# Kernel tuning notes

Measured on AMD Instinct MI355X. Metric: run time of the kernel, lower is better.

The kernel has to match this reference:

```python
import jax, jax.numpy as jnp
import numpy as np

B, D, H, V, T = 64, 1024, 1024, 32000, 20
SOS = 0  # word_to_idx['<SOS>']


def setup_inputs() -> dict:
    key = jax.random.key(0)
    ks = jax.random.split(key, 6)
    s = 0.02
    return {
        "latent_vector": jax.random.normal(ks[0], (B, D), jnp.float32),
        "W_proj": jax.random.normal(ks[1], (H, D), jnp.float32) * s,
        "b_proj": jnp.zeros((H,), jnp.float32),
        "emb": jax.random.normal(ks[2], (V, H), jnp.float32) * s,
        "W_ih": jax.random.normal(ks[3], (3 * H, H), jnp.float32) * s,
        "b_ih": jnp.zeros((3 * H,), jnp.float32),
        "W_hh": jax.random.normal(ks[4], (3 * H, H), jnp.float32) * s,
        "b_hh": jnp.zeros((3 * H,), jnp.float32),
        "W_out": jax.random.normal(ks[5], (V, H), jnp.float32) * s,
        "b_out": jnp.zeros((V,), jnp.float32),
    }


def _gru_cell(x, h, W_ih, b_ih, W_hh, b_hh):
    # PyTorch GRU cell gate math
    gi = x @ W_ih.T + b_ih  # [B, 3H]
    gh = h @ W_hh.T + b_hh  # [B, 3H]
    i_r, i_z, i_n = jnp.split(gi, 3, axis=-1)
    h_r, h_z, h_n = jnp.split(gh, 3, axis=-1)
    r = jax.nn.sigmoid(i_r + h_r)
    z = jax.nn.sigmoid(i_z + h_z)
    n = jnp.tanh(i_n + r * h_n)
    return (1.0 - z) * n + z * h


def reference(latent_vector, W_proj, b_proj, emb, W_ih, b_ih, W_hh, b_hh, W_out, b_out):
    batch = latent_vector.shape[0]
    h = latent_vector @ W_proj.T + b_proj  # init_hidden: [B, H]
    tok0 = jnp.full((batch,), SOS, dtype=jnp.int32)

    def step(carry, _):
        tok, h = carry
        x = emb[tok]                                  # embedding lookup [B, H]
        h = _gru_cell(x, h, W_ih, b_ih, W_hh, b_hh)   # GRU step
        logits = h @ W_out.T + b_out                  # [B, V]
        tok = jnp.argmax(logits, axis=-1).astype(jnp.int32)  # topk(1) greedy
        return (tok, h), tok

    (_, h_final), toks = jax.lax.scan(step, (tok0, h), None, length=T)
    # torch: stack(outputs, dim=1).squeeze() -> [B, T]; hidden -> [1, B, H]
    return toks.T, h_final[None, :, :]
```

## Files before the change

### kernel.cpp

```cpp
#include <hip/hip_runtime.h>
#include <stdint.h>

#define B_ 64
#define D_ 1024
#define H_ 1024
#define V_ 32000
#define T_ 20
#define SOS_ 0

typedef __attribute__((ext_vector_type(8))) __bf16 bf16x8;
typedef __attribute__((ext_vector_type(4))) float f32x4;

__device__ __forceinline__ uint32_t ord_of_float(float x) {
    uint32_t u = __float_as_uint(x);
    return (u & 0x80000000u) ? ~u : (u | 0x80000000u);
}

__device__ __forceinline__ unsigned long long shfl_xor_u64(unsigned long long x, int m) {
    return (unsigned long long)__shfl_xor((long long)x, m, 64);
}

__device__ __forceinline__ void split_bf16(float f, unsigned short* hi, unsigned short* lo) {
    uint32_t u = __float_as_uint(f);
    uint32_t rh = (u + 0x7FFFu + ((u >> 16) & 1u)) >> 16;
    *hi = (unsigned short)rh;
    float fl = f - __uint_as_float(rh << 16);
    uint32_t ul = __float_as_uint(fl);
    uint32_t rl = (ul + 0x7FFFu + ((ul >> 16) & 1u)) >> 16;
    *lo = (unsigned short)rl;
}

__device__ __forceinline__ void gload_lds16(const void* g, void* l) {
    __builtin_amdgcn_global_load_lds(
        (const __attribute__((address_space(1))) void*)g,
        (__attribute__((address_space(3))) void*)l, 16, 0, 0);
}

__global__ __launch_bounds__(256) void k_split_w(const float* __restrict__ src,
    unsigned short* __restrict__ hi, unsigned short* __restrict__ lo, int n4)
{
    int i = blockIdx.x * 256 + threadIdx.x;
    if (i >= n4) return;
    float4 v = ((const float4*)src)[i];
    ushort4 h, l;
    split_bf16(v.x, &h.x, &l.x);
    split_bf16(v.y, &h.y, &l.y);
    split_bf16(v.z, &h.z, &l.z);
    split_bf16(v.w, &h.w, &l.w);
    ((ushort4*)hi)[i] = h;
    ((ushort4*)lo)[i] = l;
}

__global__ __launch_bounds__(256) void k_init_hidden(
    const float* __restrict__ latent, const float* __restrict__ Wp,
    const float* __restrict__ bp, float* __restrict__ h0,
    unsigned short* __restrict__ hhi, unsigned short* __restrict__ hlo)
{
    int gw = (blockIdx.x * 256 + threadIdx.x) >> 6;
    int lane = threadIdx.x & 63;
    int j = gw >> 6;
    int b = gw & 63;
    const float4* a4 = (const float4*)(latent + b * D_);
    const float4* w4 = (const float4*)(Wp + (size_t)j * D_);
    float s = 0.f;
#pragma unroll
    for (int i = 0; i < 4; i++) {
        float4 a = a4[lane + 64 * i];
        float4 w = w4[lane + 64 * i];
        s += a.x * w.x + a.y * w.y + a.z * w.z + a.w * w.w;
    }
#pragma unroll
    for (int off = 32; off; off >>= 1) s += __shfl_down(s, off, 64);
    if (lane == 0) {
        float v = s + bp[j];
        h0[b * H_ + j] = v;
        unsigned short h_, l_;
        split_bf16(v, &h_, &l_);
        hhi[b * H_ + j] = h_;
        hlo[b * H_ + j] = l_;
    }
}

__global__ __launch_bounds__(256) void k_prep_x0(const float* __restrict__ emb,
    unsigned short* __restrict__ xhi, unsigned short* __restrict__ xlo)
{
    int b = blockIdx.x;
    int tid = threadIdx.x;
    float4 v4 = *(const float4*)(emb + (size_t)SOS_ * H_ + tid * 4);
    ushort4 h, l;
    split_bf16(v4.x, &h.x, &l.x);
    split_bf16(v4.y, &h.y, &l.y);
    split_bf16(v4.z, &h.z, &l.z);
    split_bf16(v4.w, &h.w, &l.w);
    *(ushort4*)(xhi + (size_t)b * H_ + tid * 4) = h;
    *(ushort4*)(xlo + (size_t)b * H_ + tid * 4) = l;
}

__global__ __launch_bounds__(256) void k_gates_gemm2(
    const unsigned short* __restrict__ xhi, const unsigned short* __restrict__ xlo,
    const unsigned short* __restrict__ hhi, const unsigned short* __restrict__ hlo,
    const unsigned short* __restrict__ wihh, const unsigned short* __restrict__ wihl,
    const unsigned short* __restrict__ whhh, const unsigned short* __restrict__ whhl,
    float* __restrict__ gbuf)
{
    __shared__ __align__(128) char Bsm[4][16384];
    int tid = threadIdx.x;
    int lane = tid & 63;
    int wv = tid >> 6;
    int blk = blockIdx.x;
    int jt = blk % 48;
    int rest = blk / 48;
    int half = rest & 1;
    int ks = rest >> 1;
    int kbase = ks * 256;
    int row0 = jt * 64;

    const unsigned short* Ahi_g = half ? hhi : xhi;
    const unsigned short* Alo_g = half ? hlo : xlo;
    const unsigned short* Bhi_g = half ? whhh : wihh;
    const unsigned short* Blo_g = half ? whhl : wihl;

    int r0 = wv * 8 + (lane >> 3);
    int r1 = r0 + 32;
    int kslt = (lane & 7) * 16;
    size_t so0 = (size_t)(row0 + r0) * 2048 + (size_t)(kslt ^ ((r0 & 7) << 4));
    size_t so1 = (size_t)(row0 + r1) * 2048 + (size_t)(kslt ^ ((r1 & 7) << 4));

    int mrow = wv * 16 + (lane & 15);
    int koff = (lane >> 4) * 8;
    int kb = koff * 2;

    f32x4 acc[4];
#pragma unroll
    for (int i = 0; i < 4; i++) acc[i] = (f32x4){0.f, 0.f, 0.f, 0.f};

    bf16x8 AH0[4], AH1[4], AL0[4], AL1[4];
#pragma unroll
    for (int it = 0; it < 4; it++) {
        int kc = kbase + it * 64;
        const unsigned short* ap  = Ahi_g + (size_t)mrow * 1024 + kc + koff;
        const unsigned short* alp = Alo_g + (size_t)mrow * 1024 + kc + koff;
        AH0[it] = *(const bf16x8*)ap;
        AH1[it] = *(const bf16x8*)(ap + 32);
        AL0[it] = *(const bf16x8*)alp;
        AL1[it] = *(const bf16x8*)(alp + 32);
    }
    __builtin_amdgcn_sched_barrier(0);

    auto stage = [&](int BUF, int KC) {
        const char* bh = (const char*)Bhi_g + (size_t)KC * 2;
        const char* bl = (const char*)Blo_g + (size_t)KC * 2;
        char* base = Bsm[BUF] + wv * 1024;
        gload_lds16(bh + so0, base);
        gload_lds16(bh + so1, base + 4096);
        gload_lds16(bl + so0, base + 8192);
        gload_lds16(bl + so1, base + 12288);
    };

    stage(0, kbase);
    stage(1, kbase + 64);
    stage(2, kbase + 128);
    stage(3, kbase + 192);
    __builtin_amdgcn_sched_barrier(0);

#pragma unroll
    for (int it = 0; it < 4; ++it) {
        if (it == 0)      asm volatile("s_waitcnt vmcnt(12)" ::: "memory");
        else if (it == 1) asm volatile("s_waitcnt vmcnt(8)"  ::: "memory");
        else if (it == 2) asm volatile("s_waitcnt vmcnt(4)"  ::: "memory");
        else              asm volatile("s_waitcnt vmcnt(0)"  ::: "memory");
        __builtin_amdgcn_s_barrier();
        __builtin_amdgcn_sched_barrier(0);
        const char* bhp = Bsm[it];
        const char* blp = Bsm[it] + 8192;
#pragma unroll
        for (int tv = 0; tv < 4; tv++) {
            int brow = tv * 16 + (lane & 15);
            int swz = (brow & 7) << 4;
            int ro = brow * 128;
            bf16x8 bh0 = *(const bf16x8*)(bhp + ro + (kb ^ swz));
            bf16x8 bh1 = *(const bf16x8*)(bhp + ro + ((kb + 64) ^ swz));
            bf16x8 bl0 = *(const bf16x8*)(blp + ro + (kb ^ swz));
            bf16x8 bl1 = *(const bf16x8*)(blp + ro + ((kb + 64) ^ swz));
            acc[tv] = __builtin_amdgcn_mfma_f32_16x16x32_bf16(AH0[it], bh0, acc[tv], 0, 0, 0);
            acc[tv] = __builtin_amdgcn_mfma_f32_16x16x32_bf16(AH1[it], bh1, acc[tv], 0, 0, 0);
            acc[tv] = __builtin_amdgcn_mfma_f32_16x16x32_bf16(AL0[it], bh0, acc[tv], 0, 0, 0);
            acc[tv] = __builtin_amdgcn_mfma_f32_16x16x32_bf16(AL1[it], bh1, acc[tv], 0, 0, 0);
            acc[tv] = __builtin_amdgcn_mfma_f32_16x16x32_bf16(AH0[it], bl0, acc[tv], 0, 0, 0);
            acc[tv] = __builtin_amdgcn_mfma_f32_16x16x32_bf16(AH1[it], bl1, acc[tv], 0, 0, 0);
        }
    }

    int col = lane & 15;
    int quad = lane >> 4;
    float* og = gbuf + (size_t)((ks * 2 + half) * 64) * 3072;
#pragma unroll
    for (int tv = 0; tv < 4; tv++) {
#pragma unroll
        for (int r = 0; r < 4; r++) {
            int b = wv * 16 + quad * 4 + r;
            og[(size_t)b * 3072 + jt * 64 + tv * 16 + col] = acc[tv][r];
        }
    }
}

__global__ __launch_bounds__(256) void k_gru_elem2(
    const float* __restrict__ gbuf, const float* __restrict__ bih,
    const float* __restrict__ bhh, const float* __restrict__ hprev,
    float* __restrict__ hnext, unsigned short* __restrict__ hnhi,
    unsigned short* __restrict__ hnlo)
{
    int idx = blockIdx.x * 256 + threadIdx.x;
    int b = idx >> 10;
    int j = idx & 1023;
    float ir = bih[j], hr = bhh[j];
    float iz = bih[H_ + j], hz = bhh[H_ + j];
    float in_ = bih[2 * H_ + j], hn = bhh[2 * H_ + j];
#pragma unroll
    for (int ks = 0; ks < 4; ks++) {
        const float* gi = gbuf + (size_t)(ks * 2 * 64 + b) * 3072;
        const float* gh = gbuf + (size_t)((ks * 2 + 1) * 64 + b) * 3072;
        ir += gi[j];          hr += gh[j];
        iz += gi[H_ + j];     hz += gh[H_ + j];
        in_ += gi[2 * H_ + j]; hn += gh[2 * H_ + j];
    }
    float r = 1.f / (1.f + expf(-(ir + hr)));
    float z = 1.f / (1.f + expf(-(iz + hz)));
    float n = tanhf(in_ + r * hn);
    float hp = hprev[idx];
    float v = (1.f - z) * n + z * hp;
    hnext[idx] = v;
    unsigned short h_, l_;
    split_bf16(v, &h_, &l_);
    hnhi[idx] = h_;
    hnlo[idx] = l_;
}

__global__ __launch_bounds__(256) void k_logits_argmax2(
    const unsigned short* __restrict__ hhi, const unsigned short* __restrict__ hlo,
    const unsigned short* __restrict__ wouth, const unsigned short* __restrict__ woutl,
    const float* __restrict__ bout, unsigned long long* __restrict__ partials,
    int nblk)
{
    __shared__ __align__(128) char Bsm[4][16384];
    int tid = threadIdx.x;
    int lane = tid & 63;
    int wv = tid >> 6;
    int row0 = blockIdx.x * 64;

    int r0 = wv * 8 + (lane >> 3);
    int r1 = r0 + 32;
    int kslt = (lane & 7) * 16;
    size_t so0 = (size_t)(row0 + r0) * 2048 + (size_t)(kslt ^ ((r0 & 7) << 4));
    size_t so1 = (size_t)(row0 + r1) * 2048 + (size_t)(kslt ^ ((r1 & 7) << 4));

    int mrow = wv * 16 + (lane & 15);
    int koff = (lane >> 4) * 8;
    int kb = koff * 2;

    f32x4 acc[4];
#pragma unroll
    for (int i = 0; i < 4; i++) acc[i] = (f32x4){0.f, 0.f, 0.f, 0.f};

    auto stage = [&](int BUF, int KC) {
        const char* bh = (const char*)wouth + (size_t)KC * 2;
        const char* bl = (const char*)woutl + (size_t)KC * 2;
        char* base = Bsm[BUF] + wv * 1024;
        gload_lds16(bh + so0, base);
        gload_lds16(bh + so1, base + 4096);
        gload_lds16(bl + so0, base + 8192);
        gload_lds16(bl + so1, base + 12288);
    };

    struct AF { bf16x8 h0, h1, l0, l1; };
    auto loadA = [&](int kc) {
        AF f;
        const unsigned short* ap  = hhi + (size_t)mrow * 1024 + kc + koff;
        const unsigned short* alp = hlo + (size_t)mrow * 1024 + kc + koff;
        f.h0 = *(const bf16x8*)ap;
        f.h1 = *(const bf16x8*)(ap + 32);
        f.l0 = *(const bf16x8*)alp;
        f.l1 = *(const bf16x8*)(alp + 32);
        return f;
    };
    auto mmaBlk = [&](const AF& a, const char* bhp, const char* blp) {
#pragma unroll
        for (int tv = 0; tv < 4; tv++) {
            int brow = tv * 16 + (lane & 15);
            int swz = (brow & 7) << 4;
            int ro = brow * 128;
            bf16x8 bh0 = *(const bf16x8*)(bhp + ro + (kb ^ swz));
            bf16x8 bh1 = *(const bf16x8*)(bhp + ro + ((kb + 64) ^ swz));
            bf16x8 bl0 = *(const bf16x8*)(blp + ro + (kb ^ swz));
            bf16x8 bl1 = *(const bf16x8*)(blp + ro + ((kb + 64) ^ swz));
            acc[tv] = __builtin_amdgcn_mfma_f32_16x16x32_bf16(a.h0, bh0, acc[tv], 0, 0, 0);
            acc[tv] = __builtin_amdgcn_mfma_f32_16x16x32_bf16(a.h1, bh1, acc[tv], 0, 0, 0);
            acc[tv] = __builtin_amdgcn_mfma_f32_16x16x32_bf16(a.l0, bh0, acc[tv], 0, 0, 0);
            acc[tv] = __builtin_amdgcn_mfma_f32_16x16x32_bf16(a.l1, bh1, acc[tv], 0, 0, 0);
            acc[tv] = __builtin_amdgcn_mfma_f32_16x16x32_bf16(a.h0, bl0, acc[tv], 0, 0, 0);
            acc[tv] = __builtin_amdgcn_mfma_f32_16x16x32_bf16(a.h1, bl1, acc[tv], 0, 0, 0);
        }
    };

    stage(0, 0);
    stage(1, 64);
    stage(2, 128);
    __builtin_amdgcn_sched_barrier(0);
    AF Ae = loadA(0);
    AF Ao;
    __builtin_amdgcn_sched_barrier(0);

    for (int it2 = 0; it2 < 16; it2 += 2) {
        if (it2 == 0 || it2 == 14) asm volatile("s_waitcnt vmcnt(0)" ::: "memory");
        else                       asm volatile("s_waitcnt vmcnt(4)" ::: "memory");
        __builtin_amdgcn_s_barrier();
        __builtin_amdgcn_sched_barrier(0);
        Ao = loadA((it2 + 1) * 64);
        __builtin_amdgcn_sched_barrier(0);
        if (it2 <= 12) stage((it2 + 3) & 3, (it2 + 3) * 64);
        __builtin_amdgcn_sched_barrier(0);
        mmaBlk(Ae, Bsm[it2 & 3], Bsm[it2 & 3] + 8192);

        if (it2 + 1 >= 14) asm volatile("s_waitcnt vmcnt(0)" ::: "memory");
        else               asm volatile("s_waitcnt vmcnt(4)" ::: "memory");
        __builtin_amdgcn_s_barrier();
        __builtin_amdgcn_sched_barrier(0);
        if (it2 + 2 < 16) Ae = loadA((it2 + 2) * 64);
        __builtin_amdgcn_sched_barrier(0);
        if (it2 + 1 <= 12) stage((it2 + 4) & 3, (it2 + 4) * 64);
        __builtin_amdgcn_sched_barrier(0);
        mmaBlk(Ao, Bsm[(it2 + 1) & 3], Bsm[(it2 + 1) & 3] + 8192);
    }

    int col = lane & 15;
    int quad = lane >> 4;
    unsigned long long kmax[4] = {0ull, 0ull, 0ull, 0ull};
#pragma unroll
    for (int tv = 0; tv < 4; tv++) {
        int v = row0 + tv * 16 + col;
        float bo = bout[v];
#pragma unroll
        for (int r = 0; r < 4; r++) {
            float lg = acc[tv][r] + bo;
            unsigned long long key = ((unsigned long long)ord_of_float(lg) << 32)
                                   | (unsigned long long)(0x7FFFFFFFu - (uint32_t)v);
            if (key > kmax[r]) kmax[r] = key;
        }
    }
#pragma unroll
    for (int r = 0; r < 4; r++) {
        unsigned long long k = kmax[r];
#pragma unroll
        for (int off = 1; off < 16; off <<= 1) {
            unsigned long long o = shfl_xor_u64(k, off);
            if (o > k) k = o;
        }
        kmax[r] = k;
    }
    if (col == 0) {
#pragma unroll
        for (int r = 0; r < 4; r++) {
            int b = wv * 16 + quad * 4 + r;
            partials[(size_t)b * nblk + blockIdx.x] = kmax[r];
        }
    }
}

__global__ __launch_bounds__(256) void k_token2(
    const unsigned long long* __restrict__ partials, int nblk,
    int* __restrict__ tok, float* __restrict__ out_tokens, int t,
    const float* __restrict__ emb,
    unsigned short* __restrict__ xhi, unsigned short* __restrict__ xlo)
{
    __shared__ int s_tok;
    int b = blockIdx.x;
    int tid = threadIdx.x;
    if (tid < 64) {
        unsigned long long k = 0ull;
        for (int i = tid; i < nblk; i += 64) {
            unsigned long long p = partials[(size_t)b * nblk + i];
            if (p > k) k = p;
        }
#pragma unroll
        for (int off = 32; off; off >>= 1) {
            unsigned long long o = shfl_xor_u64(k, off);
            if (o > k) k = o;
        }
        if (tid == 0) {
            int v = (int)(0x7FFFFFFFu - (uint32_t)(k & 0xFFFFFFFFull));
            tok[b] = v;
            out_tokens[b * T_ + t] = (float)v;
            s_tok = v;
        }
    }
    __syncthreads();
    int row = s_tok;
    float4 v4 = *(const float4*)(emb + (size_t)row * H_ + tid * 4);
    ushort4 h, l;
    split_bf16(v4.x, &h.x, &l.x);
    split_bf16(v4.y, &h.y, &l.y);
    split_bf16(v4.z, &h.z, &l.z);
    split_bf16(v4.w, &h.w, &l.w);
    *(ushort4*)(xhi + (size_t)b * H_ + tid * 4) = h;
    *(ushort4*)(xlo + (size_t)b * H_ + tid * 4) = l;
}

__global__ __launch_bounds__(256) void k_copy_h(const float* __restrict__ h,
                                               float* __restrict__ out)
{
    int i = (blockIdx.x * 256 + threadIdx.x) * 4;
    *(float4*)(out + i) = *(const float4*)(h + i);
}

extern "C" void kernel_launch(void* const* d_in, const int* in_sizes, int n_in,
                              void* d_out, int out_size, void* d_ws, size_t ws_size,
                              hipStream_t stream)
{
    const float* latent = (const float*)d_in[0];
    const float* Wp     = (const float*)d_in[1];
    const float* bp     = (const float*)d_in[2];
    const float* emb    = (const float*)d_in[3];
    const float* Wih    = (const float*)d_in[4];
    const float* bih    = (const float*)d_in[5];
    const float* Whh    = (const float*)d_in[6];
    const float* bhh    = (const float*)d_in[7];
    const float* Wout   = (const float*)d_in[8];
    const float* bout   = (const float*)d_in[9];
    float* out = (float*)d_out;

    char* ws = (char*)d_ws;
    float* h0   = (float*)(ws + 0);
    float* h1   = (float*)(ws + 262144);
    int* tok    = (int*)(ws + 524288);
    unsigned long long* partials = (unsigned long long*)(ws + 525312);
    float* gbuf = (float*)(ws + 787456);
    unsigned short* hhi0 = (unsigned short*)(ws + 7078912);
    unsigned short* hlo0 = (unsigned short*)(ws + 7209984);
    unsigned short* hhi1 = (unsigned short*)(ws + 7341056);
    unsigned short* hlo1 = (unsigned short*)(ws + 7472128);
    unsigned short* xhi  = (unsigned short*)(ws + 7603200);
    unsigned short* xlo  = (unsigned short*)(ws + 7734272);
    unsigned short* wihh = (unsigned short*)(ws + 7865344);
    unsigned short* wihl = (unsigned short*)(ws + 14156800);
    unsigned short* whhh = (unsigned short*)(ws + 20448256);
    unsigned short* whhl = (unsigned short*)(ws + 26739712);
    unsigned short* wouth = (unsigned short*)(ws + 33031168);
    unsigned short* woutl = (unsigned short*)(ws + 98567168);

    const int NBLK = V_ / 64;

    k_split_w<<<3072, 256, 0, stream>>>(Wih, wihh, wihl, 3 * H_ * H_ / 4);
    k_split_w<<<3072, 256, 0, stream>>>(Whh, whhh, whhl, 3 * H_ * H_ / 4);
    k_split_w<<<32000, 256, 0, stream>>>(Wout, wouth, woutl, V_ * H_ / 4);

    k_init_hidden<<<16384, 256, 0, stream>>>(latent, Wp, bp, h0, hhi0, hlo0);
    k_prep_x0<<<64, 256, 0, stream>>>(emb, xhi, xlo);

    float* hp = h0;  unsigned short* hphi = hhi0;  unsigned short* hplo = hlo0;
    float* hn = h1;  unsigned short* hnhi = hhi1;  unsigned short* hnlo = hlo1;
    for (int t = 0; t < T_; t++) {
        k_gates_gemm2<<<384, 256, 0, stream>>>(xhi, xlo, hphi, hplo,
                                               wihh, wihl, whhh, whhl, gbuf);
        k_gru_elem2<<<256, 256, 0, stream>>>(gbuf, bih, bhh, hp, hn, hnhi, hnlo);
        k_logits_argmax2<<<NBLK, 256, 0, stream>>>(hnhi, hnlo, wouth, woutl,
                                                   bout, partials, NBLK);
        k_token2<<<B_, 256, 0, stream>>>(partials, NBLK, tok, out, t, emb, xhi, xlo);
        { float* tf = hp; hp = hn; hn = tf; }
        { unsigned short* ts = hphi; hphi = hnhi; hnhi = ts; }
        { unsigned short* ts = hplo; hplo = hnlo; hnlo = ts; }
    }
    k_copy_h<<<64, 256, 0, stream>>>(hp, out + B_ * T_);
}
```

Baseline: 1.185 ms.

## Fuse GRU gate GEMM with elementwise update via permuted weight layout; MFMA init projection

```diff
diff --git a/kernel.cpp b/kernel.cpp
--- a/kernel.cpp
+++ b/kernel.cpp
@@ -51,34 +51,24 @@
     ((ushort4*)lo)[i] = l;
 }
 
-__global__ __launch_bounds__(256) void k_init_hidden(
-    const float* __restrict__ latent, const float* __restrict__ Wp,
-    const float* __restrict__ bp, float* __restrict__ h0,
-    unsigned short* __restrict__ hhi, unsigned short* __restrict__ hlo)
-{
-    int gw = (blockIdx.x * 256 + threadIdx.x) >> 6;
-    int lane = threadIdx.x & 63;
-    int j = gw >> 6;
-    int b = gw & 63;
-    const float4* a4 = (const float4*)(latent + b * D_);
-    const float4* w4 = (const float4*)(Wp + (size_t)j * D_);
-    float s = 0.f;
-#pragma unroll
-    for (int i = 0; i < 4; i++) {
-        float4 a = a4[lane + 64 * i];
-        float4 w = w4[lane + 64 * i];
-        s += a.x * w.x + a.y * w.y + a.z * w.z + a.w * w.w;
-    }
-#pragma unroll
-    for (int off = 32; off; off >>= 1) s += __shfl_down(s, off, 64);
-    if (lane == 0) {
-        float v = s + bp[j];
-        h0[b * H_ + j] = v;
-        unsigned short h_, l_;
-        split_bf16(v, &h_, &l_);
-        hhi[b * H_ + j] = h_;
-        hlo[b * H_ + j] = l_;
-    }
+__global__ __launch_bounds__(256) void k_split_w_perm(const float* __restrict__ src,
+    unsigned short* __restrict__ hi, unsigned short* __restrict__ lo)
+{
+    int rp = blockIdx.x;
+    int jt = rp / 48;
+    int rem = rp % 48;
+    int g = rem >> 4;
+    int jl = rem & 15;
+    int orig = g * H_ + jt * 16 + jl;
+    int c4 = threadIdx.x * 4;
+    float4 v = *(const float4*)(src + (size_t)orig * H_ + c4);
+    ushort4 h, l;
+    split_bf16(v.x, &h.x, &l.x);
+    split_bf16(v.y, &h.y, &l.y);
+    split_bf16(v.z, &h.z, &l.z);
+    split_bf16(v.w, &h.w, &l.w);
+    *(ushort4*)(hi + (size_t)rp * H_ + c4) = h;
+    *(ushort4*)(lo + (size_t)rp * H_ + c4) = l;
 }
 
 __global__ __launch_bounds__(256) void k_prep_x0(const float* __restrict__ emb,
@@ -96,29 +86,17 @@
     *(ushort4*)(xlo + (size_t)b * H_ + tid * 4) = l;
 }
 
-__global__ __launch_bounds__(256) void k_gates_gemm2(
-    const unsigned short* __restrict__ xhi, const unsigned short* __restrict__ xlo,
-    const unsigned short* __restrict__ hhi, const unsigned short* __restrict__ hlo,
-    const unsigned short* __restrict__ wihh, const unsigned short* __restrict__ wihl,
-    const unsigned short* __restrict__ whhh, const unsigned short* __restrict__ whhl,
-    float* __restrict__ gbuf)
+__global__ __launch_bounds__(256) void k_init_gemm(
+    const unsigned short* __restrict__ lathi, const unsigned short* __restrict__ latlo,
+    const unsigned short* __restrict__ wphi, const unsigned short* __restrict__ wplo,
+    const float* __restrict__ bp, float* __restrict__ h0,
+    unsigned short* __restrict__ hhi, unsigned short* __restrict__ hlo)
 {
     __shared__ __align__(128) char Bsm[4][16384];
     int tid = threadIdx.x;
     int lane = tid & 63;
     int wv = tid >> 6;
-    int blk = blockIdx.x;
-    int jt = blk % 48;
-    int rest = blk / 48;
-    int half = rest & 1;
-    int ks = rest >> 1;
-    int kbase = ks * 256;
-    int row0 = jt * 64;
-
-    const unsigned short* Ahi_g = half ? hhi : xhi;
-    const unsigned short* Alo_g = half ? hlo : xlo;
-    const unsigned short* Bhi_g = half ? whhh : wihh;
-    const unsigned short* Blo_g = half ? whhl : wihl;
+    int row0 = blockIdx.x * 64;
 
     int r0 = wv * 8 + (lane >> 3);
     int r1 = r0 + 32;
@@ -134,22 +112,9 @@
 #pragma unroll
     for (int i = 0; i < 4; i++) acc[i] = (f32x4){0.f, 0.f, 0.f, 0.f};
 
-    bf16x8 AH0[4], AH1[4], AL0[4], AL1[4];
-#pragma unroll
-    for (int it = 0; it < 4; it++) {
-        int kc = kbase + it * 64;
-        const unsigned short* ap  = Ahi_g + (size_t)mrow * 1024 + kc + koff;
-        const unsigned short* alp = Alo_g + (size_t)mrow * 1024 + kc + koff;
-        AH0[it] = *(const bf16x8*)ap;
-        AH1[it] = *(const bf16x8*)(ap + 32);
-        AL0[it] = *(const bf16x8*)alp;
-        AL1[it] = *(const bf16x8*)(alp + 32);
-    }
-    __builtin_amdgcn_sched_barrier(0);
-
     auto stage = [&](int BUF, int KC) {
-        const char* bh = (const char*)Bhi_g + (size_t)KC * 2;
-        const char* bl = (const char*)Blo_g + (size_t)KC * 2;
+        const char* bh = (const char*)wphi + (size_t)KC * 2;
+        const char* bl = (const char*)wplo + (size_t)KC * 2;
         char* base = Bsm[BUF] + wv * 1024;
         gload_lds16(bh + so0, base);
         gload_lds16(bh + so1, base + 4096);
@@ -157,22 +122,25 @@
         gload_lds16(bl + so1, base + 12288);
     };
 
-    stage(0, kbase);
-    stage(1, kbase + 64);
-    stage(2, kbase + 128);
-    stage(3, kbase + 192);
-    __builtin_amdgcn_sched_barrier(0);
-
-#pragma unroll
-    for (int it = 0; it < 4; ++it) {
-        if (it == 0)      asm volatile("s_waitcnt vmcnt(12)" ::: "memory");
-        else if (it == 1) asm volatile("s_waitcnt vmcnt(8)"  ::: "memory");
-        else if (it == 2) asm volatile("s_waitcnt vmcnt(4)"  ::: "memory");
-        else              asm volatile("s_waitcnt vmcnt(0)"  ::: "memory");
+    stage(0, 0);
+    stage(1, 64);
+    stage(2, 128);
+
+    for (int it = 0; it < 16; ++it) {
+        if (it == 0)      asm volatile("s_waitcnt vmcnt(8)"  ::: "memory");
+        else if (it == 1) asm volatile("s_waitcnt vmcnt(12)" ::: "memory");
+        else              asm volatile("s_waitcnt vmcnt(16)" ::: "memory");
         __builtin_amdgcn_s_barrier();
         __builtin_amdgcn_sched_barrier(0);
-        const char* bhp = Bsm[it];
-        const char* blp = Bsm[it] + 8192;
+        int kc = it * 64;
+        const unsigned short* ap  = lathi + (size_t)mrow * 1024 + kc + koff;
+        const unsigned short* alp = latlo + (size_t)mrow * 1024 + kc + koff;
+        bf16x8 ah0 = *(const bf16x8*)ap;
+        bf16x8 ah1 = *(const bf16x8*)(ap + 32);
+        bf16x8 al0 = *(const bf16x8*)alp;
+        bf16x8 al1 = *(const bf16x8*)(alp + 32);
+        const char* bhp = Bsm[it & 3];
+        const char* blp = Bsm[it & 3] + 8192;
 #pragma unroll
         for (int tv = 0; tv < 4; tv++) {
             int brow = tv * 16 + (lane & 15);
@@ -182,58 +150,167 @@
             bf16x8 bh1 = *(const bf16x8*)(bhp + ro + ((kb + 64) ^ swz));
             bf16x8 bl0 = *(const bf16x8*)(blp + ro + (kb ^ swz));
             bf16x8 bl1 = *(const bf16x8*)(blp + ro + ((kb + 64) ^ swz));
-            acc[tv] = __builtin_amdgcn_mfma_f32_16x16x32_bf16(AH0[it], bh0, acc[tv], 0, 0, 0);
-            acc[tv] = __builtin_amdgcn_mfma_f32_16x16x32_bf16(AH1[it], bh1, acc[tv], 0, 0, 0);
-            acc[tv] = __builtin_amdgcn_mfma_f32_16x16x32_bf16(AL0[it], bh0, acc[tv], 0, 0, 0);
-            acc[tv] = __builtin_amdgcn_mfma_f32_16x16x32_bf16(AL1[it], bh1, acc[tv], 0, 0, 0);
-            acc[tv] = __builtin_amdgcn_mfma_f32_16x16x32_bf16(AH0[it], bl0, acc[tv], 0, 0, 0);
-            acc[tv] = __builtin_amdgcn_mfma_f32_16x16x32_bf16(AH1[it], bl1, acc[tv], 0, 0, 0);
-        }
+            acc[tv] = __builtin_amdgcn_mfma_f32_16x16x32_bf16(ah0, bh0, acc[tv], 0, 0, 0);
+            acc[tv] = __builtin_amdgcn_mfma_f32_16x16x32_bf16(ah1, bh1, acc[tv], 0, 0, 0);
+            acc[tv] = __builtin_amdgcn_mfma_f32_16x16x32_bf16(al0, bh0, acc[tv], 0, 0, 0);
+            acc[tv] = __builtin_amdgcn_mfma_f32_16x16x32_bf16(al1, bh1, acc[tv], 0, 0, 0);
+            acc[tv] = __builtin_amdgcn_mfma_f32_16x16x32_bf16(ah0, bl0, acc[tv], 0, 0, 0);
+            acc[tv] = __builtin_amdgcn_mfma_f32_16x16x32_bf16(ah1, bl1, acc[tv], 0, 0, 0);
+        }
+        if (it <= 12) stage((it + 3) & 3, (it + 3) * 64);
     }
 
     int col = lane & 15;
     int quad = lane >> 4;
-    float* og = gbuf + (size_t)((ks * 2 + half) * 64) * 3072;
 #pragma unroll
     for (int tv = 0; tv < 4; tv++) {
+        int j = row0 + tv * 16 + col;
+        float bo = bp[j];
 #pragma unroll
         for (int r = 0; r < 4; r++) {
             int b = wv * 16 + quad * 4 + r;
-            og[(size_t)b * 3072 + jt * 64 + tv * 16 + col] = acc[tv][r];
-        }
-    }
-}
-
-__global__ __launch_bounds__(256) void k_gru_elem2(
-    const float* __restrict__ gbuf, const float* __restrict__ bih,
-    const float* __restrict__ bhh, const float* __restrict__ hprev,
-    float* __restrict__ hnext, unsigned short* __restrict__ hnhi,
-    unsigned short* __restrict__ hnlo)
-{
-    int idx = blockIdx.x * 256 + threadIdx.x;
-    int b = idx >> 10;
-    int j = idx & 1023;
-    float ir = bih[j], hr = bhh[j];
-    float iz = bih[H_ + j], hz = bhh[H_ + j];
-    float in_ = bih[2 * H_ + j], hn = bhh[2 * H_ + j];
-#pragma unroll
-    for (int ks = 0; ks < 4; ks++) {
-        const float* gi = gbuf + (size_t)(ks * 2 * 64 + b) * 3072;
-        const float* gh = gbuf + (size_t)((ks * 2 + 1) * 64 + b) * 3072;
-        ir += gi[j];          hr += gh[j];
-        iz += gi[H_ + j];     hz += gh[H_ + j];
-        in_ += gi[2 * H_ + j]; hn += gh[2 * H_ + j];
-    }
-    float r = 1.f / (1.f + expf(-(ir + hr)));
-    float z = 1.f / (1.f + expf(-(iz + hz)));
-    float n = tanhf(in_ + r * hn);
-    float hp = hprev[idx];
-    float v = (1.f - z) * n + z * hp;
-    hnext[idx] = v;
-    unsigned short h_, l_;
-    split_bf16(v, &h_, &l_);
-    hnhi[idx] = h_;
-    hnlo[idx] = l_;
+            float v = acc[tv][r] + bo;
+            h0[(size_t)b * H_ + j] = v;
+            unsigned short h_, l_;
+            split_bf16(v, &h_, &l_);
+            hhi[(size_t)b * H_ + j] = h_;
+            hlo[(size_t)b * H_ + j] = l_;
+        }
+    }
+}
+
+struct AF8 { bf16x8 h[4]; bf16x8 l[4]; };
+
+#define GMMA(AV, ACC, BUFPTR) do {                                              \
+    const char* _bp = (BUFPTR);                                                 \
+    _Pragma("unroll")                                                           \
+    for (int tv = 0; tv < 3; tv++) {                                            \
+        int brow = tv * 16 + (lane & 15);                                       \
+        int sw = (brow & 15) << 4;                                              \
+        const char* rh = _bp + brow * 256;                                      \
+        const char* rl = _bp + 12288 + brow * 256;                              \
+        _Pragma("unroll")                                                       \
+        for (int ks = 0; ks < 4; ks++) {                                        \
+            bf16x8 bh = *(const bf16x8*)(rh + ((ks * 64 + kb) ^ sw));           \
+            bf16x8 bl = *(const bf16x8*)(rl + ((ks * 64 + kb) ^ sw));           \
+            ACC[tv] = __builtin_amdgcn_mfma_f32_16x16x32_bf16(AV.h[ks], bh, ACC[tv], 0, 0, 0); \
+            ACC[tv] = __builtin_amdgcn_mfma_f32_16x16x32_bf16(AV.l[ks], bh, ACC[tv], 0, 0, 0); \
+            ACC[tv] = __builtin_amdgcn_mfma_f32_16x16x32_bf16(AV.h[ks], bl, ACC[tv], 0, 0, 0); \
+        }                                                                       \
+    }                                                                           \
+} while (0)
+
+__global__ __launch_bounds__(256) void k_gru_step(
+    const unsigned short* __restrict__ xhi, const unsigned short* __restrict__ xlo,
+    const unsigned short* __restrict__ hphi, const unsigned short* __restrict__ hplo,
+    const unsigned short* __restrict__ wihh, const unsigned short* __restrict__ wihl,
+    const unsigned short* __restrict__ whhh, const unsigned short* __restrict__ whhl,
+    const float* __restrict__ bih, const float* __restrict__ bhh,
+    const float* __restrict__ hprev, float* __restrict__ hnext,
+    unsigned short* __restrict__ hnhi, unsigned short* __restrict__ hnlo)
+{
+    __shared__ __align__(128) char Bsm[4][24576];
+    int tid = threadIdx.x;
+    int lane = tid & 63;
+    int wv = tid >> 6;
+    int jt = blockIdx.x;
+    int prow0 = jt * 48;
+
+    int mrow = wv * 16 + (lane & 15);
+    int koff = (lane >> 4) * 8;
+    int kb = koff * 2;
+
+    f32x4 acc_h[3], acc_i[3];
+#pragma unroll
+    for (int i = 0; i < 3; i++) {
+        acc_h[i] = (f32x4){0.f, 0.f, 0.f, 0.f};
+        acc_i[i] = (f32x4){0.f, 0.f, 0.f, 0.f};
+    }
+
+    auto stageG = [&](int s) {
+        const unsigned short* PH = (s & 1) ? wihh : whhh;
+        const unsigned short* PL = (s & 1) ? wihl : whhl;
+        size_t kcb = (size_t)((s >> 1) * 128) * 2;
+#pragma unroll
+        for (int m = 0; m < 6; m++) {
+            int c = wv + m * 4;
+            const unsigned short* P = (c < 12) ? PH : PL;
+            int row = (c % 12) * 4 + (lane >> 4);
+            int slot = (lane & 15) * 16;
+            size_t off = (size_t)(prow0 + row) * 2048 + kcb
+                       + (size_t)(slot ^ ((row & 15) << 4));
+            gload_lds16((const char*)P + off, Bsm[s & 3] + c * 1024);
+        }
+    };
+
+    auto loadA8 = [&](const unsigned short* Phi, const unsigned short* Plo, int kc) {
+        AF8 f;
+#pragma unroll
+        for (int ks = 0; ks < 4; ks++) {
+            f.h[ks] = *(const bf16x8*)(Phi + (size_t)mrow * 1024 + kc + ks * 32 + koff);
+            f.l[ks] = *(const bf16x8*)(Plo + (size_t)mrow * 1024 + kc + ks * 32 + koff);
+        }
+        return f;
+    };
+
+    stageG(0);
+    stageG(1);
+    stageG(2);
+    __builtin_amdgcn_sched_barrier(0);
+    AF8 Ah = loadA8(hphi, hplo, 0);
+    AF8 Ao;
+    __builtin_amdgcn_sched_barrier(0);
+
+    for (int i2 = 0; i2 < 16; i2 += 2) {
+        int kc = (i2 >> 1) * 128;
+        if (i2 == 0)       asm volatile("s_waitcnt vmcnt(20)" ::: "memory");
+        else if (i2 == 14) asm volatile("s_waitcnt vmcnt(22)" ::: "memory");
+        else               asm volatile("s_waitcnt vmcnt(28)" ::: "memory");
+        __builtin_amdgcn_s_barrier();
+        __builtin_amdgcn_sched_barrier(0);
+        Ao = loadA8(xhi, xlo, kc);
+        __builtin_amdgcn_sched_barrier(0);
+        if (i2 + 3 < 16) stageG(i2 + 3);
+        __builtin_amdgcn_sched_barrier(0);
+        GMMA(Ah, acc_h, Bsm[i2 & 3]);
+
+        if (i2 + 1 == 15) asm volatile("s_waitcnt vmcnt(16)" ::: "memory");
+        else              asm volatile("s_waitcnt vmcnt(28)" ::: "memory");
+        __builtin_amdgcn_s_barrier();
+        __builtin_amdgcn_sched_barrier(0);
+        if (i2 + 2 < 16) Ah = loadA8(hphi, hplo, kc + 128);
+        __builtin_amdgcn_sched_barrier(0);
+        if (i2 + 4 < 16) stageG(i2 + 4);
+        __builtin_amdgcn_sched_barrier(0);
+        GMMA(Ao, acc_i, Bsm[(i2 + 1) & 3]);
+    }
+
+    int jl = lane & 15;
+    int quad = lane >> 4;
+    int j = jt * 16 + jl;
+    float bir = bih[j],        bhr = bhh[j];
+    float biz = bih[H_ + j],   bhz = bhh[H_ + j];
+    float bin = bih[2 * H_ + j], bhn = bhh[2 * H_ + j];
+#pragma unroll
+    for (int r = 0; r < 4; r++) {
+        int b = wv * 16 + quad * 4 + r;
+        float ir = acc_i[0][r] + bir;
+        float iz = acc_i[1][r] + biz;
+        float in_ = acc_i[2][r] + bin;
+        float hr = acc_h[0][r] + bhr;
+        float hz = acc_h[1][r] + bhz;
+        float hn = acc_h[2][r] + bhn;
+        float rg = 1.f / (1.f + expf(-(ir + hr)));
+        float z  = 1.f / (1.f + expf(-(iz + hz)));
+        float n  = tanhf(in_ + rg * hn);
+        float hpv = hprev[(size_t)b * H_ + j];
+        float v = (1.f - z) * n + z * hpv;
+        hnext[(size_t)b * H_ + j] = v;
+        unsigned short h_, l_;
+        split_bf16(v, &h_, &l_);
+        hnhi[(size_t)b * H_ + j] = h_;
+        hnlo[(size_t)b * H_ + j] = l_;
+    }
 }
 
 __global__ __launch_bounds__(256) void k_logits_argmax2(
@@ -433,35 +510,40 @@
     float* h1   = (float*)(ws + 262144);
     int* tok    = (int*)(ws + 524288);
     unsigned long long* partials = (unsigned long long*)(ws + 525312);
-    float* gbuf = (float*)(ws + 787456);
-    unsigned short* hhi0 = (unsigned short*)(ws + 7078912);
-    unsigned short* hlo0 = (unsigned short*)(ws + 7209984);
-    unsigned short* hhi1 = (unsigned short*)(ws + 7341056);
-    unsigned short* hlo1 = (unsigned short*)(ws + 7472128);
-    unsigned short* xhi  = (unsigned short*)(ws + 7603200);
-    unsigned short* xlo  = (unsigned short*)(ws + 7734272);
-    unsigned short* wihh = (unsigned short*)(ws + 7865344);
-    unsigned short* wihl = (unsigned short*)(ws + 14156800);
-    unsigned short* whhh = (unsigned short*)(ws + 20448256);
-    unsigned short* whhl = (unsigned short*)(ws + 26739712);
-    unsigned short* wouth = (unsigned short*)(ws + 33031168);
-    unsigned short* woutl = (unsigned short*)(ws + 98567168);
+    unsigned short* hhi0 = (unsigned short*)(ws + 787456);
+    unsigned short* hlo0 = (unsigned short*)(ws + 918528);
+    unsigned short* hhi1 = (unsigned short*)(ws + 1049600);
+    unsigned short* hlo1 = (unsigned short*)(ws + 1180672);
+    unsigned short* xhi  = (unsigned short*)(ws + 1311744);
+    unsigned short* xlo  = (unsigned short*)(ws + 1442816);
+    unsigned short* lathi = (unsigned short*)(ws + 1573888);
+    unsigned short* latlo = (unsigned short*)(ws + 1704960);
+    unsigned short* wphi  = (unsigned short*)(ws + 1836032);
+    unsigned short* wplo  = (unsigned short*)(ws + 3933184);
+    unsigned short* wihh = (unsigned short*)(ws + 6030336);
+    unsigned short* wihl = (unsigned short*)(ws + 12321792);
+    unsigned short* whhh = (unsigned short*)(ws + 18613248);
+    unsigned short* whhl = (unsigned short*)(ws + 24904704);
+    unsigned short* wouth = (unsigned short*)(ws + 31196160);
+    unsigned short* woutl = (unsigned short*)(ws + 96732160);
 
     const int NBLK = V_ / 64;
 
-    k_split_w<<<3072, 256, 0, stream>>>(Wih, wihh, wihl, 3 * H_ * H_ / 4);
-    k_split_w<<<3072, 256, 0, stream>>>(Whh, whhh, whhl, 3 * H_ * H_ / 4);
+    k_split_w_perm<<<3072, 256, 0, stream>>>(Wih, wihh, wihl);
+    k_split_w_perm<<<3072, 256, 0, stream>>>(Whh, whhh, whhl);
     k_split_w<<<32000, 256, 0, stream>>>(Wout, wouth, woutl, V_ * H_ / 4);
-
-    k_init_hidden<<<16384, 256, 0, stream>>>(latent, Wp, bp, h0, hhi0, hlo0);
+    k_split_w<<<1024, 256, 0, stream>>>(Wp, wphi, wplo, H_ * D_ / 4);
+    k_split_w<<<64, 256, 0, stream>>>(latent, lathi, latlo, B_ * D_ / 4);
+
+    k_init_gemm<<<16, 256, 0, stream>>>(lathi, latlo, wphi, wplo, bp, h0, hhi0, hlo0);
     k_prep_x0<<<64, 256, 0, stream>>>(emb, xhi, xlo);
 
     float* hp = h0;  unsigned short* hphi = hhi0;  unsigned short* hplo = hlo0;
     float* hn = h1;  unsigned short* hnhi = hhi1;  unsigned short* hnlo = hlo1;
     for (int t = 0; t < T_; t++) {
-        k_gates_gemm2<<<384, 256, 0, stream>>>(xhi, xlo, hphi, hplo,
-                                               wihh, wihl, whhh, whhl, gbuf);
-        k_gru_elem2<<<256, 256, 0, stream>>>(gbuf, bih, bhh, hp, hn, hnhi, hnlo);
+        k_gru_step<<<64, 256, 0, stream>>>(xhi, xlo, hphi, hplo,
+                                           wihh, wihl, whhh, whhl,
+                                           bih, bhh, hp, hn, hnhi, hnlo);
         k_logits_argmax2<<<NBLK, 256, 0, stream>>>(hnhi, hnlo, wouth, woutl,
                                                    bout, partials, NBLK);
         k_token2<<<B_, 256, 0, stream>>>(partials, NBLK, tok, out, t, emb, xhi, xlo);
```

Result: slower. 1.476 ms (+24.5%).

## Replace scalar init-hidden projection with split-bf16 MFMA GEMM and deepen logits pipeline

Applied to the files above, without the earlier changes.

```diff
diff --git a/kernel.cpp b/kernel.cpp
--- a/kernel.cpp
+++ b/kernel.cpp
@@ -51,36 +51,6 @@
     ((ushort4*)lo)[i] = l;
 }
 
-__global__ __launch_bounds__(256) void k_init_hidden(
-    const float* __restrict__ latent, const float* __restrict__ Wp,
-    const float* __restrict__ bp, float* __restrict__ h0,
-    unsigned short* __restrict__ hhi, unsigned short* __restrict__ hlo)
-{
-    int gw = (blockIdx.x * 256 + threadIdx.x) >> 6;
-    int lane = threadIdx.x & 63;
-    int j = gw >> 6;
-    int b = gw & 63;
-    const float4* a4 = (const float4*)(latent + b * D_);
-    const float4* w4 = (const float4*)(Wp + (size_t)j * D_);
-    float s = 0.f;
-#pragma unroll
-    for (int i = 0; i < 4; i++) {
-        float4 a = a4[lane + 64 * i];
-        float4 w = w4[lane + 64 * i];
-        s += a.x * w.x + a.y * w.y + a.z * w.z + a.w * w.w;
-    }
-#pragma unroll
-    for (int off = 32; off; off >>= 1) s += __shfl_down(s, off, 64);
-    if (lane == 0) {
-        float v = s + bp[j];
-        h0[b * H_ + j] = v;
-        unsigned short h_, l_;
-        split_bf16(v, &h_, &l_);
-        hhi[b * H_ + j] = h_;
-        hlo[b * H_ + j] = l_;
-    }
-}
-
 __global__ __launch_bounds__(256) void k_prep_x0(const float* __restrict__ emb,
     unsigned short* __restrict__ xhi, unsigned short* __restrict__ xlo)
 {
@@ -94,6 +64,99 @@
     split_bf16(v4.w, &h.w, &l.w);
     *(ushort4*)(xhi + (size_t)b * H_ + tid * 4) = h;
     *(ushort4*)(xlo + (size_t)b * H_ + tid * 4) = l;
+}
+
+__global__ __launch_bounds__(256) void k_init_gemm(
+    const unsigned short* __restrict__ lathi, const unsigned short* __restrict__ latlo,
+    const unsigned short* __restrict__ wphi, const unsigned short* __restrict__ wplo,
+    const float* __restrict__ bp, float* __restrict__ h0,
+    unsigned short* __restrict__ hhi, unsigned short* __restrict__ hlo)
+{
+    __shared__ __align__(128) char Bsm[4][16384];
+    int tid = threadIdx.x;
+    int lane = tid & 63;
+    int wv = tid >> 6;
+    int row0 = blockIdx.x * 64;
+
+    int r0 = wv * 8 + (lane >> 3);
+    int r1 = r0 + 32;
+    int kslt = (lane & 7) * 16;
+    size_t so0 = (size_t)(row0 + r0) * 2048 + (size_t)(kslt ^ ((r0 & 7) << 4));
+    size_t so1 = (size_t)(row0 + r1) * 2048 + (size_t)(kslt ^ ((r1 & 7) << 4));
+
+    int mrow = wv * 16 + (lane & 15);
+    int koff = (lane >> 4) * 8;
+    int kb = koff * 2;
+
+    f32x4 acc[4];
+#pragma unroll
+    for (int i = 0; i < 4; i++) acc[i] = (f32x4){0.f, 0.f, 0.f, 0.f};
+
+    auto stage = [&](int BUF, int KC) {
+        const char* bh = (const char*)wphi + (size_t)KC * 2;
+        const char* bl = (const char*)wplo + (size_t)KC * 2;
+        char* base = Bsm[BUF] + wv * 1024;
+        gload_lds16(bh + so0, base);
+        gload_lds16(bh + so1, base + 4096);
+        gload_lds16(bl + so0, base + 8192);
+        gload_lds16(bl + so1, base + 12288);
+    };
+
+    stage(0, 0);
+    stage(1, 64);
+    stage(2, 128);
+
+    for (int it = 0; it < 16; ++it) {
+        if (it == 0)      asm volatile("s_waitcnt vmcnt(8)"  ::: "memory");
+        else if (it == 1) asm volatile("s_waitcnt vmcnt(12)" ::: "memory");
+        else              asm volatile("s_waitcnt vmcnt(16)" ::: "memory");
+        __builtin_amdgcn_s_barrier();
+        __builtin_amdgcn_sched_barrier(0);
+        int kc = it * 64;
+        const unsigned short* ap  = lathi + (size_t)mrow * 1024 + kc + koff;
+        const unsigned short* alp = latlo + (size_t)mrow * 1024 + kc + koff;
+        bf16x8 ah0 = *(const bf16x8*)ap;
+        bf16x8 ah1 = *(const bf16x8*)(ap + 32);
+        bf16x8 al0 = *(const bf16x8*)alp;
+        bf16x8 al1 = *(const bf16x8*)(alp + 32);
+        const char* bhp = Bsm[it & 3];
+        const char* blp = Bsm[it & 3] + 8192;
+#pragma unroll
+        for (int tv = 0; tv < 4; tv++) {
+            int brow = tv * 16 + (lane & 15);
+            int swz = (brow & 7) << 4;
+            int ro = brow * 128;
+            bf16x8 bh0 = *(const bf16x8*)(bhp + ro + (kb ^ swz));
+            bf16x8 bh1 = *(const bf16x8*)(bhp + ro + ((kb + 64) ^ swz));
+            bf16x8 bl0 = *(const bf16x8*)(blp + ro + (kb ^ swz));
+            bf16x8 bl1 = *(const bf16x8*)(blp + ro + ((kb + 64) ^ swz));
+            acc[tv] = __builtin_amdgcn_mfma_f32_16x16x32_bf16(ah0, bh0, acc[tv], 0, 0, 0);
+            acc[tv] = __builtin_amdgcn_mfma_f32_16x16x32_bf16(ah1, bh1, acc[tv], 0, 0, 0);
+            acc[tv] = __builtin_amdgcn_mfma_f32_16x16x32_bf16(al0, bh0, acc[tv], 0, 0, 0);
+            acc[tv] = __builtin_amdgcn_mfma_f32_16x16x32_bf16(al1, bh1, acc[tv], 0, 0, 0);
+            acc[tv] = __builtin_amdgcn_mfma_f32_16x16x32_bf16(ah0, bl0, acc[tv], 0, 0, 0);
+            acc[tv] = __builtin_amdgcn_mfma_f32_16x16x32_bf16(ah1, bl1, acc[tv], 0, 0, 0);
+        }
+        if (it <= 12) stage((it + 3) & 3, (it + 3) * 64);
+    }
+
+    int col = lane & 15;
+    int quad = lane >> 4;
+#pragma unroll
+    for (int tv = 0; tv < 4; tv++) {
+        int j = row0 + tv * 16 + col;
+        float bo = bp[j];
+#pragma unroll
+        for (int r = 0; r < 4; r++) {
+            int b = wv * 16 + quad * 4 + r;
+            float v = acc[tv][r] + bo;
+            h0[(size_t)b * H_ + j] = v;
+            unsigned short h_, l_;
+            split_bf16(v, &h_, &l_);
+            hhi[(size_t)b * H_ + j] = h_;
+            hlo[(size_t)b * H_ + j] = l_;
+        }
+    }
 }
 
 __global__ __launch_bounds__(256) void k_gates_gemm2(
@@ -236,7 +299,7 @@
     hnlo[idx] = l_;
 }
 
-__global__ __launch_bounds__(256) void k_logits_argmax2(
+__global__ __launch_bounds__(256) void k_logits_argmax3(
     const unsigned short* __restrict__ hhi, const unsigned short* __restrict__ hlo,
     const unsigned short* __restrict__ wouth, const unsigned short* __restrict__ woutl,
     const float* __restrict__ bout, unsigned long long* __restrict__ partials,
@@ -306,30 +369,24 @@
     stage(1, 64);
     stage(2, 128);
     __builtin_amdgcn_sched_barrier(0);
-    AF Ae = loadA(0);
-    AF Ao;
+    AF A[3];
+    A[0] = loadA(0);
+    A[1] = loadA(64);
     __builtin_amdgcn_sched_barrier(0);
 
-    for (int it2 = 0; it2 < 16; it2 += 2) {
-        if (it2 == 0 || it2 == 14) asm volatile("s_waitcnt vmcnt(0)" ::: "memory");
-        else                       asm volatile("s_waitcnt vmcnt(4)" ::: "memory");
+#pragma unroll
+    for (int it = 0; it < 16; ++it) {
+        if (it == 15)                 asm volatile("s_waitcnt vmcnt(0)"  ::: "memory");
+        else if (it == 0)             asm volatile("s_waitcnt vmcnt(4)"  ::: "memory");
+        else if (it == 1 || it == 14) asm volatile("s_waitcnt vmcnt(8)"  ::: "memory");
+        else                          asm volatile("s_waitcnt vmcnt(12)" ::: "memory");
         __builtin_amdgcn_s_barrier();
         __builtin_amdgcn_sched_barrier(0);
-        Ao = loadA((it2 + 1) * 64);
+        if (it + 2 < 16) A[(it + 2) % 3] = loadA((it + 2) * 64);
         __builtin_amdgcn_sched_barrier(0);
-        if (it2 <= 12) stage((it2 + 3) & 3, (it2 + 3) * 64);
+        if (it + 3 < 16) stage((it + 3) & 3, (it + 3) * 64);
         __builtin_amdgcn_sched_barrier(0);
-        mmaBlk(Ae, Bsm[it2 & 3], Bsm[it2 & 3] + 8192);
-
-        if (it2 + 1 >= 14) asm volatile("s_waitcnt vmcnt(0)" ::: "memory");
-        else               asm volatile("s_waitcnt vmcnt(4)" ::: "memory");
-        __builtin_amdgcn_s_barrier();
-        __builtin_amdgcn_sched_barrier(0);
-        if (it2 + 2 < 16) Ae = loadA((it2 + 2) * 64);
-        __builtin_amdgcn_sched_barrier(0);
-        if (it2 + 1 <= 12) stage((it2 + 4) & 3, (it2 + 4) * 64);
-        __builtin_amdgcn_sched_barrier(0);
-        mmaBlk(Ao, Bsm[(it2 + 1) & 3], Bsm[(it2 + 1) & 3] + 8192);
+        mmaBlk(A[it % 3], Bsm[it & 3], Bsm[it & 3] + 8192);
     }
 
     int col = lane & 15;
@@ -440,20 +497,26 @@
     unsigned short* hlo1 = (unsigned short*)(ws + 7472128);
     unsigned short* xhi  = (unsigned short*)(ws + 7603200);
     unsigned short* xlo  = (unsigned short*)(ws + 7734272);
-    unsigned short* wihh = (unsigned short*)(ws + 7865344);
-    unsigned short* wihl = (unsigned short*)(ws + 14156800);
-    unsigned short* whhh = (unsigned short*)(ws + 20448256);
-    unsigned short* whhl = (unsigned short*)(ws + 26739712);
-    unsigned short* wouth = (unsigned short*)(ws + 33031168);
-    unsigned short* woutl = (unsigned short*)(ws + 98567168);
+    unsigned short* lathi = (unsigned short*)(ws + 7865344);
+    unsigned short* latlo = (unsigned short*)(ws + 7996416);
+    unsigned short* wphi  = (unsigned short*)(ws + 8127488);
+    unsigned short* wplo  = (unsigned short*)(ws + 10224640);
+    unsigned short* wihh = (unsigned short*)(ws + 12321792);
+    unsigned short* wihl = (unsigned short*)(ws + 18613248);
+    unsigned short* whhh = (unsigned short*)(ws + 24904704);
+    unsigned short* whhl = (unsigned short*)(ws + 31196160);
+    unsigned short* wouth = (unsigned short*)(ws + 37487616);
+    unsigned short* woutl = (unsigned short*)(ws + 103023616);
 
     const int NBLK = V_ / 64;
 
     k_split_w<<<3072, 256, 0, stream>>>(Wih, wihh, wihl, 3 * H_ * H_ / 4);
     k_split_w<<<3072, 256, 0, stream>>>(Whh, whhh, whhl, 3 * H_ * H_ / 4);
     k_split_w<<<32000, 256, 0, stream>>>(Wout, wouth, woutl, V_ * H_ / 4);
-
-    k_init_hidden<<<16384, 256, 0, stream>>>(latent, Wp, bp, h0, hhi0, hlo0);
+    k_split_w<<<1024, 256, 0, stream>>>(Wp, wphi, wplo, H_ * D_ / 4);
+    k_split_w<<<64, 256, 0, stream>>>(latent, lathi, latlo, B_ * D_ / 4);
+
+    k_init_gemm<<<16, 256, 0, stream>>>(lathi, latlo, wphi, wplo, bp, h0, hhi0, hlo0);
     k_prep_x0<<<64, 256, 0, stream>>>(emb, xhi, xlo);
 
     float* hp = h0;  unsigned short* hphi = hhi0;  unsigned short* hplo = hlo0;
@@ -462,7 +525,7 @@
         k_gates_gemm2<<<384, 256, 0, stream>>>(xhi, xlo, hphi, hplo,
                                                wihh, wihl, whhh, whhl, gbuf);
         k_gru_elem2<<<256, 256, 0, stream>>>(gbuf, bih, bhh, hp, hn, hnhi, hnlo);
-        k_logits_argmax2<<<NBLK, 256, 0, stream>>>(hnhi, hnlo, wouth, woutl,
+        k_logits_argmax3<<<NBLK, 256, 0, stream>>>(hnhi, hnlo, wouth, woutl,
                                                    bout, partials, NBLK);
         k_token2<<<B_, 256, 0, stream>>>(partials, NBLK, tok, out, t, emb, xhi, xlo);
         { float* tf = hp; hp = hn; hn = tf; }
```

New measurement: 1.204 ms. About the same (+1.5%).
